# Kernel optimization log

Hardware: AMD Instinct MI355X
Metric: run time of the kernel (lower is better)

Reference implementation:

```python
import jax, jax.numpy as jnp
import numpy as np

N, E, B = 50000, 200000, 512
F0, H1, C2, EMB = 78, 10, 128, 128
SEQ, VOCAB, NF, KW = 1000, 26, 32, 8
LOUT = EMB - KW + 1  # 121


def setup_inputs() -> dict:
    key = jax.random.key(0)
    ks = jax.random.split(key, 20)
    nrm = lambda k, s: jax.random.normal(k, s, jnp.float32) * 0.05
    return dict(
        x=jax.random.normal(ks[0], (N, F0), jnp.float32),
        edge_index=jax.random.randint(ks[1], (2, E), 0, N),
        batch=(jnp.arange(N) * B) // N,  # balanced sorted node->graph ids, all segments non-empty
        target=jax.random.randint(ks[2], (B, SEQ), 0, VOCAB),
        W1=nrm(ks[3], (F0, H1 * F0)), a_src1=nrm(ks[4], (H1, F0)), a_dst1=nrm(ks[5], (H1, F0)), b1=jnp.zeros((H1 * F0,), jnp.float32),
        W2=nrm(ks[6], (H1 * F0, C2)), a_src2=nrm(ks[7], (1, C2)), a_dst2=nrm(ks[8], (1, C2)), b2=jnp.zeros((C2,), jnp.float32),
        fc_g1_w=nrm(ks[9], (C2, C2)), fc_g1_b=jnp.zeros((C2,), jnp.float32),
        emb=nrm(ks[10], (VOCAB, EMB)),
        conv_w=nrm(ks[11], (NF, SEQ, KW)), conv_b=jnp.zeros((NF,), jnp.float32),
        fc_xt_w=nrm(ks[12], (NF * LOUT, C2)), fc_xt_b=jnp.zeros((C2,), jnp.float32),
        fc1_w=nrm(ks[13], (2 * C2, 1024)), fc1_b=jnp.zeros((1024,), jnp.float32),
        fc2_w=nrm(ks[14], (1024, 256)), fc2_b=jnp.zeros((256,), jnp.float32),
        out_w=nrm(ks[15], (256, 1)), out_b=jnp.zeros((1,), jnp.float32),
    )


def gat_conv(x, src, dst, W, a_src, a_dst, b, heads):
    # PyG GATConv (eval mode): project, per-edge attn logits, segment softmax over dst, scatter-add
    n = x.shape[0]
    c = W.shape[1] // heads
    h = (x @ W).reshape(n, heads, c)                 # [N,H,C]
    al_s = (h * a_src).sum(-1)                       # [N,H]
    al_d = (h * a_dst).sum(-1)
    al = jax.nn.leaky_relu(al_s[src] + al_d[dst], 0.2)   # [E',H]
    amax = jax.ops.segment_max(al, dst, num_segments=n)
    ex = jnp.exp(al - amax[dst])
    den = jax.ops.segment_sum(ex, dst, num_segments=n)
    alpha = ex / (den[dst] + 1e-16)
    out = jax.ops.segment_sum(h[src] * alpha[:, :, None], dst, num_segments=n)  # [N,H,C]
    return out.reshape(n, heads * c) + b


def reference(x, edge_index, batch, target, W1, a_src1, a_dst1, b1, W2, a_src2, a_dst2, b2,
              fc_g1_w, fc_g1_b, emb, conv_w, conv_b, fc_xt_w, fc_xt_b,
              fc1_w, fc1_b, fc2_w, fc2_b, out_w, out_b):
    n = x.shape[0]
    loops = jnp.arange(n)
    src = jnp.concatenate([edge_index[0], loops])    # add self loops (PyG default)
    dst = jnp.concatenate([edge_index[1], loops])
    h = jax.nn.elu(gat_conv(x, src, dst, W1, a_src1, a_dst1, b1, H1))
    h = jax.nn.relu(gat_conv(h, src, dst, W2, a_src2, a_dst2, b2, 1))
    g = jax.ops.segment_max(h, batch, num_segments=B)            # global max pool per graph
    g = jax.nn.relu(g @ fc_g1_w + fc_g1_b)                       # [B,128]
    e = emb[target]                                              # [B,1000,128]
    conv = jax.lax.conv_general_dilated(e, conv_w, (1,), 'VALID',
                                        dimension_numbers=('NCH', 'OIH', 'NCH'))
    conv = jax.nn.relu(conv + conv_b[None, :, None])             # [B,32,121]
    xt = conv.reshape(B, NF * LOUT) @ fc_xt_w + fc_xt_b          # [B,128]
    xc = jnp.concatenate([g, xt], axis=1)                        # [B,256]
    xc = jax.nn.relu(xc @ fc1_w + fc1_b)
    xc = jax.nn.relu(xc @ fc2_w + fc2_b)
    return xc @ out_w + out_b                                    # [B,1]
```

## Files before the change

### kernel.cpp

```cpp
#include <hip/hip_runtime.h>
#include <hip/hip_bf16.h>

#define N_NODES 50000
#define N_EDGES 200000
#define BGRAPHS 512
#define F0c 78
#define H1c 10
#define HC1 780
#define HSTR 832
#define C2c 128
#define SEQc 1000
#define VOCABc 26
#define NFc 32
#define KWc 8
#define LOUTc 121
#define EMBc 128
#define KX 96
#define KXT 3872
#define MROWS 13312
#define KM 1024
#define W2TF_N (25*8*64*8)
#define NSCANB 196

typedef __attribute__((ext_vector_type(8))) short short8;
typedef __attribute__((ext_vector_type(4))) float f32x4;
typedef unsigned short u16;

static constexpr size_t alignup(size_t x) { return (x + 255) & ~size_t(255); }

static constexpr size_t A_HBUF = 0;
static constexpr size_t A_OUT1 = alignup(A_HBUF + size_t(N_NODES)*HSTR*2);
static constexpr size_t A_H2   = alignup(A_OUT1 + size_t(N_NODES)*HSTR*2);
static constexpr size_t A_W2T  = alignup(A_H2   + size_t(N_NODES)*C2c*4);
static constexpr size_t A_ALS1 = alignup(A_W2T  + size_t(C2c)*HSTR*2);
static constexpr size_t A_ALD1 = alignup(A_ALS1 + size_t(N_NODES)*H1c*4);
static constexpr size_t A_ALS2 = alignup(A_ALD1 + size_t(N_NODES)*H1c*4);
static constexpr size_t A_ALD2 = alignup(A_ALS2 + size_t(N_NODES)*4);
static constexpr size_t A_DEG  = alignup(A_ALD2 + size_t(N_NODES)*4);
static constexpr size_t A_OFFS = alignup(A_DEG  + size_t(N_NODES)*4);
static constexpr size_t A_CUR  = alignup(A_OFFS + size_t(N_NODES+1)*4);
static constexpr size_t A_CSRC = alignup(A_CUR  + size_t(N_NODES)*4);
static constexpr size_t A_XC   = alignup(A_CSRC + size_t(N_EDGES+N_NODES)*4);
static constexpr size_t A_Y1   = alignup(A_XC   + size_t(BGRAPHS)*256*4);
static constexpr size_t A_BOFF = alignup(A_Y1   + size_t(BGRAPHS)*1024*4);
static constexpr size_t A_BPAD = alignup(A_BOFF + size_t(BGRAPHS)*(VOCABc+1)*4);
static constexpr size_t A_WXT  = alignup(A_BPAD + size_t(HSTR)*4);
static constexpr size_t A_FXP  = alignup(A_WXT  + size_t(C2c)*KXT*2);
static constexpr size_t A_W1HP = alignup(A_FXP  + size_t(11)*BGRAPHS*C2c*4);
static constexpr size_t A_WSD  = alignup(A_W1HP + size_t(10)*80*96*2);
static constexpr size_t A_CWT  = alignup(A_WSD  + size_t(2)*H1c*F0c*4);
static constexpr size_t A_END  = alignup(A_CWT  + size_t(2)*256*KM*2);
static_assert(W2TF_N*2 <= size_t(C2c)*HSTR*2, "w2tf fits old slot");
static_assert((NSCANB+1)*4 <= BGRAPHS*(VOCABc+1)*4, "bsum fits A_BOFF slot");

static constexpr size_t A_HFIN = A_HBUF;
static constexpr size_t A_AMAT = alignup(A_HFIN + size_t(N_NODES)*C2c*4);
static constexpr size_t A_CVO  = alignup(A_AMAT + size_t(MROWS)*256*4);
static constexpr size_t A_M    = alignup(A_CVO  + size_t(BGRAPHS)*KXT*2);
static_assert(A_M + size_t(MROWS)*KM*2 <= size_t(N_NODES)*HSTR*2, "alias A overflow");
static constexpr size_t A_XPAD = A_OUT1;
static_assert(size_t(N_NODES)*KX*2 <= size_t(N_NODES)*HSTR*2, "alias B overflow");

__device__ __forceinline__ float bflo(unsigned u) { return __uint_as_float(u << 16); }
__device__ __forceinline__ float bfhi(unsigned u) { return __uint_as_float(u & 0xffff0000u); }
__device__ __forceinline__ u16 f2bf(float v) {
    __hip_bfloat16 b = __float2bfloat16(v);
    return *(u16*)&b;
}

#define GLOAD16(g, l) __builtin_amdgcn_global_load_lds( \
    (const __attribute__((address_space(1))) void*)(g), \
    (__attribute__((address_space(3))) void*)(l), 16, 0, 0)

__global__ void k_prep(const float* __restrict__ x, const float* __restrict__ W1,
                       const float* __restrict__ W2, const float* __restrict__ b1,
                       const float* __restrict__ fcxt_w, const float* __restrict__ conv_w,
                       const float* __restrict__ a_src1, const float* __restrict__ a_dst1,
                       __hip_bfloat16* __restrict__ xpad, __hip_bfloat16* __restrict__ w1hp,
                       u16* __restrict__ w2tf, float* __restrict__ bpad,
                       u16* __restrict__ wxt, float* __restrict__ wsd,
                       u16* __restrict__ cwt, int* __restrict__ deg) {
    int i = blockIdx.x*256 + threadIdx.x;
    const int R0 = N_NODES;
    const int R1 = R0 + N_NODES*KX;
    const int R2 = R1 + 10*80*96;
    const int R3 = R2 + W2TF_N;
    const int R4 = R3 + HSTR;
    const int R5 = R4 + C2c*KXT;
    const int R6 = R5 + 2*H1c*F0c;
    const int R7 = R6 + 256*KM;
    if (i < R0) {
        deg[i] = 1;
    } else if (i < R1) {
        int t = i - R0; int n = t / KX, c = t - n*KX;
        xpad[t] = __float2bfloat16(c < F0c ? x[(size_t)n*F0c + c] : 0.f);
    } else if (i < R2) {
        int t = i - R1; int hh = t / 7680, rem = t - hh*7680;
        int j = rem / 96, k = rem - j*96;
        w1hp[t] = __float2bfloat16((j < F0c && k < F0c) ? W1[(size_t)k*HC1 + hh*F0c + j] : 0.f);
    } else if (i < R3) {
        int t = i - R2; int frag = t >> 3, tt = t & 7;
        int m16 = frag & 15, quad = (frag >> 4) & 3, cbg = (frag >> 6) & 7, kstep = frag >> 9;
        int col = cbg*16 + m16;
        int k = kstep*32 + quad*8 + tt;
        int hh = k / 80, cc = k - hh*80;
        w2tf[t] = f2bf((cc < F0c) ? W2[(size_t)(hh*F0c + cc)*C2c + col] : 0.f);
    } else if (i < R4) {
        int p = i - R3; int hh = p / 80, cc = p - hh*80;
        bpad[p] = (hh < H1c && cc < F0c) ? b1[hh*F0c + cc] : 0.f;
    } else if (i < R5) {
        int t = i - R4; int frag = t >> 3, tt = t & 7;
        int lane = frag & 63, m16 = lane & 15, quad = lane >> 4;
        int ct = (frag >> 6) & 7, kt = frag >> 9;
        wxt[t] = f2bf(fcxt_w[(size_t)(kt*32 + quad*8 + tt)*C2c + (ct*16 + m16)]);
    } else if (i < R6) {
        int t = i - R5; int sd = t / (H1c*F0c), rem = t - sd*(H1c*F0c);
        int hh = rem / F0c, c = rem - hh*F0c;
        const float* a = sd ? a_dst1 : a_src1;
        float v = 0.f;
        for (int j = 0; j < F0c; j++) v += W1[(size_t)c*HC1 + hh*F0c + j] * a[hh*F0c + j];
        wsd[t] = v;
    } else if (i < R7) {
        int t = i - R6; int col = t >> 10, ii = t & (KM-1);
        int o = col >> 3, k = col & 7;
        float v = (ii < SEQc) ? conv_w[((size_t)o*SEQc + ii)*KWc + k] : 0.f;
        u16 h = f2bf(v);
        float hv = __uint_as_float((unsigned)h << 16);
        cwt[(size_t)col*KM + ii] = h;
        cwt[(size_t)256*KM + (size_t)col*KM + ii] = f2bf(v - hv);
    }
}
#define PREP_TOTAL (N_NODES + N_NODES*KX + 10*80*96 + W2TF_N + HSTR + C2c*KXT + 2*H1c*F0c + 256*KM)

__global__ void k_count(const int* __restrict__ ei, int* deg) {
    int i = blockIdx.x*256 + threadIdx.x;
    if (i < N_EDGES) atomicAdd(&deg[ei[N_EDGES + i]], 1);
}
__global__ void k_scan1(const int* __restrict__ deg, int* __restrict__ offs,
                        int* __restrict__ bsum, int n) {
    int b = blockIdx.x, tid = threadIdx.x, lane = tid & 63, wid = tid >> 6;
    int i = b*256 + tid;
    int v0 = (i < n) ? deg[i] : 0;
    int v = v0;
    for (int d = 1; d < 64; d <<= 1) { int t = __shfl_up(v, d, 64); if (lane >= d) v += t; }
    __shared__ int ws[4];
    if (lane == 63) ws[wid] = v;
    __syncthreads();
    if (tid == 0) {
        int r = 0;
        #pragma unroll
        for (int w = 0; w < 4; w++) { int t = ws[w]; ws[w] = r; r += t; }
        bsum[b] = r;
    }
    __syncthreads();
    if (i < n) offs[i] = ws[wid] + (v - v0);
}
__global__ void k_scan2(int* __restrict__ bsum, int nb) {
    __shared__ int s[NSCANB];
    int tid = threadIdx.x;
    for (int i = tid; i < nb; i += 256) s[i] = bsum[i];
    __syncthreads();
    if (tid == 0) {
        int r = 0;
        for (int b = 0; b < nb; b++) { int t = s[b]; s[b] = r; r += t; }
        bsum[nb] = r;
    }
    __syncthreads();
    for (int i = tid; i < nb; i += 256) bsum[i] = s[i];
}
__global__ void k_scan3(const int* __restrict__ bsum, int* __restrict__ offs,
                        int* __restrict__ cur, int n, int nb) {
    int b = blockIdx.x, i = b*256 + threadIdx.x;
    if (i < n) {
        int o = offs[i] + bsum[b];
        offs[i] = o; cur[i] = o;
    } else if (i == n) {
        offs[n] = bsum[nb];
    }
}
__global__ void k_fill(const int* __restrict__ ei, int* cur, int* __restrict__ csrc) {
    int i = blockIdx.x*256 + threadIdx.x;
    if (i < N_EDGES) {
        int s = ei[i], d = ei[N_EDGES + i];
        int p = atomicAdd(&cur[d], 1);
        csrc[p] = s;
    } else if (i < N_EDGES + N_NODES) {
        int n = i - N_EDGES;
        int p = atomicAdd(&cur[n], 1);
        csrc[p] = n;
    }
}
__global__ void k_sortcsr(const int* __restrict__ offs, int* __restrict__ csrc) {
    int n = blockIdx.x*256 + threadIdx.x;
    if (n >= N_NODES) return;
    int s = offs[n], e = offs[n+1];
    for (int i = s + 1; i < e; i++) {
        int v = csrc[i];
        int j = i - 1;
        while (j >= s && csrc[j] > v) { csrc[j+1] = csrc[j]; j--; }
        csrc[j+1] = v;
    }
}

__global__ void k_att1x(const float* __restrict__ x, const float* __restrict__ wsd,
                        float* __restrict__ als, float* __restrict__ ald) {
    int i = blockIdx.x*256 + threadIdx.x;
    if (i >= N_NODES*H1c) return;
    int n = i / H1c, hh = i - n*H1c;
    const float* xr = x + (size_t)n*F0c;
    const float* ws = wsd + hh*F0c;
    const float* wd = wsd + H1c*F0c + hh*F0c;
    float s1 = 0.f, s2 = 0.f;
    for (int c = 0; c < F0c; c++) { float v = xr[c]; s1 += v*ws[c]; s2 += v*wd[c]; }
    als[i] = s1; ald[i] = s2;
}

__global__ void k_agg1x(const unsigned* __restrict__ xpu, const float* __restrict__ als,
                        const float* __restrict__ ald, const int* __restrict__ offs,
                        const int* __restrict__ csrc, unsigned* __restrict__ xaggu) {
    constexpr int H = H1c;
    int dn = blockIdx.x, lane = threadIdx.x;
    int s = offs[dn], e = offs[dn+1], deg = e - s;
    __shared__ float wexp[64*H];
    __shared__ int   ssrc[64];
    __shared__ float ms[H], dinv_s[H];

    if (deg <= 64) {
        if (lane < deg) ssrc[lane] = csrc[s + lane];
        __syncthreads();
        for (int idx = lane; idx < deg*H; idx += 64) {
            int j = idx / H, hh = idx - j*H;
            float al = als[(size_t)ssrc[j]*H + hh] + ald[(size_t)dn*H + hh];
            wexp[idx] = (al >= 0.f) ? al : 0.2f*al;
        }
        __syncthreads();
        if (lane < H) {
            float m = -1e30f;
            for (int j = 0; j < deg; j++) m = fmaxf(m, wexp[j*H + lane]);
            float den = 0.f;
            for (int j = 0; j < deg; j++) den += __expf(wexp[j*H + lane] - m);
            ms[lane] = m; dinv_s[lane] = 1.f/(den + 1e-16f);
        }
        __syncthreads();
        for (int idx = lane; idx < deg*H; idx += 64) {
            int hh = idx % H;
            wexp[idx] = __expf(wexp[idx] - ms[hh]) * dinv_s[hh];
        }
        __syncthreads();
        if (lane < 40) {
            float accL[H], accH[H];
            #pragma unroll
            for (int hh = 0; hh < H; hh++) { accL[hh] = 0.f; accH[hh] = 0.f; }
            int j = 0;
            for (; j + 1 < deg; j += 2) {
                unsigned ua = xpu[(size_t)ssrc[j]*48 + lane];
                unsigned ub = xpu[(size_t)ssrc[j+1]*48 + lane];
                float a0 = bflo(ua), a1 = bfhi(ua), b0 = bflo(ub), b1 = bfhi(ub);
                #pragma unroll
                for (int hh = 0; hh < H; hh++) {
                    float wA = wexp[j*H + hh], wB = wexp[(j+1)*H + hh];
                    accL[hh] += wA*a0 + wB*b0;
                    accH[hh] += wA*a1 + wB*b1;
                }
            }
            if (j < deg) {
                unsigned ua = xpu[(size_t)ssrc[j]*48 + lane];
                float a0 = bflo(ua), a1 = bfhi(ua);
                #pragma unroll
                for (int hh = 0; hh < H; hh++) {
                    float wA = wexp[j*H + hh];
                    accL[hh] += wA*a0;
                    accH[hh] += wA*a1;
                }
            }
            #pragma unroll
            for (int hh = 0; hh < H; hh++) {
                unsigned p = (unsigned)f2bf(accL[hh]) | ((unsigned)f2bf(accH[hh]) << 16);
                xaggu[((size_t)dn*H + hh)*40 + lane] = p;
            }
        }
    } else {
        if (lane < H) {
            float adv = ald[(size_t)dn*H + lane];
            float m = -1e30f;
            for (int j = s; j < e; j++) {
                float al = als[(size_t)csrc[j]*H + lane] + adv;
                al = (al >= 0.f) ? al : 0.2f*al;
                m = fmaxf(m, al);
            }
            float den = 0.f;
            for (int j = s; j < e; j++) {
                float al = als[(size_t)csrc[j]*H + lane] + adv;
                al = (al >= 0.f) ? al : 0.2f*al;
                den += __expf(al - m);
            }
            ms[lane] = m; dinv_s[lane] = 1.f/(den + 1e-16f);
        }
        __syncthreads();
        if (lane < 40) {
            float accL[H], accH[H];
            #pragma unroll
            for (int hh = 0; hh < H; hh++) { accL[hh] = 0.f; accH[hh] = 0.f; }
            for (int j = s; j < e; j++) {
                int sj = csrc[j];
                unsigned ua = xpu[(size_t)sj*48 + lane];
                float a0 = bflo(ua), a1 = bfhi(ua);
                #pragma unroll
                for (int hh = 0; hh < H; hh++) {
                    float al = als[(size_t)sj*H + hh] + ald[(size_t)dn*H + hh];
                    al = (al >= 0.f) ? al : 0.2f*al;
                    float a = __expf(al - ms[hh]) * dinv_s[hh];
                    accL[hh] += a*a0;
                    accH[hh] += a*a1;
                }
            }
            #pragma unroll
            for (int hh = 0; hh < H; hh++) {
                unsigned p = (unsigned)f2bf(accL[hh]) | ((unsigned)f2bf(accH[hh]) << 16);
                xaggu[((size_t)dn*H + hh)*40 + lane] = p;
            }
        }
    }
}

__global__ void __launch_bounds__(256, 8)
k_fuse12(const short* __restrict__ xagg, const short* __restrict__ w1hp,
         const float* __restrict__ bpad, const short* __restrict__ w2tf,
         const float* __restrict__ a_src2, const float* __restrict__ a_dst2,
         float* __restrict__ Cout, float* __restrict__ als2, float* __restrict__ ald2) {
    __shared__ __attribute__((aligned(16))) short As[16*832];
    int tid = threadIdx.x;
    int wave = tid >> 6, lane = tid & 63;
    int m16 = lane & 15, quad = lane >> 4;
    int blockrow = blockIdx.x * 16;

    {
        int hg = wave;
        int rowc = min(blockrow + m16, N_NODES-1);
        for (int hh = hg; hh < H1c; hh += 4) {
            const short8* arow = (const short8*)(xagg + ((size_t)rowc*H1c + hh)*80);
            f32x4 acc1[5];
            #pragma unroll
            for (int ct = 0; ct < 5; ct++) acc1[ct] = (f32x4){0.f,0.f,0.f,0.f};
            #pragma unroll
            for (int kt = 0; kt < 3; kt++) {
                short8 af = arow[kt*4 + quad];
                #pragma unroll
                for (int ct = 0; ct < 5; ct++) {
                    const short8* brow = (const short8*)(w1hp + (size_t)(hh*80 + ct*16 + m16)*96);
                    acc1[ct] = __builtin_amdgcn_mfma_f32_16x16x32_bf16(af, brow[kt*4 + quad],
                                                                      acc1[ct], 0, 0, 0);
                }
            }
            #pragma unroll
            for (int ct = 0; ct < 5; ct++) {
                int col = hh*80 + ct*16 + m16;
                float bv = bpad[col];
                #pragma unroll
                for (int r = 0; r < 4; r++) {
                    int rl = quad*4 + r;
                    float v = acc1[ct][r] + bv;
                    v = (v > 0.f) ? v : (__expf(v) - 1.f);
                    *(u16*)((char*)As + rl*1664 + ((col*2) ^ ((rl & 7) << 4))) = f2bf(v);
                }
            }
        }
    }
    __syncthreads();

    int cg = wave;
    f32x4 acc[2];
    acc[0] = (f32x4){0.f,0.f,0.f,0.f};
    acc[1] = (f32x4){0.f,0.f,0.f,0.f};
    int S = (m16 & 7) << 4;
    const char* asRow = (const char*)As + (size_t)m16*1664;
    const short8* bp = (const short8*)w2tf;
    #pragma unroll 5
    for (int kstep = 0; kstep < 25; kstep++) {
        short8 af = *(const short8*)(asRow + ((kstep*64 + quad*16) ^ S));
        short8 b0 = bp[(size_t)(kstep*8 + cg*2    )*64 + lane];
        short8 b1 = bp[(size_t)(kstep*8 + cg*2 + 1)*64 + lane];
        acc[0] = __builtin_amdgcn_mfma_f32_16x16x32_bf16(af, b0, acc[0], 0, 0, 0);
        acc[1] = __builtin_amdgcn_mfma_f32_16x16x32_bf16(af, b1, acc[1], 0, 0, 0);
    }

    float asv[2], adv[2];
    #pragma unroll
    for (int ct = 0; ct < 2; ct++) {
        asv[ct] = a_src2[cg*32 + ct*16 + m16];
        adv[ct] = a_dst2[cg*32 + ct*16 + m16];
    }
    #pragma unroll
    for (int ct = 0; ct < 2; ct++) {
        int col = cg*32 + ct*16 + m16;
        #pragma unroll
        for (int r = 0; r < 4; r++) {
            int orow = blockrow + quad*4 + r;
            if (orow < N_NODES) Cout[(size_t)orow*C2c + col] = acc[ct][r];
        }
    }

    __syncthreads();
    float* sred  = (float*)As;
    float* sredd = sred + 64;
    #pragma unroll
    for (int r = 0; r < 4; r++) {
        float s1 = 0.f, s2 = 0.f;
        #pragma unroll
        for (int ct = 0; ct < 2; ct++) { s1 += acc[ct][r]*asv[ct]; s2 += acc[ct][r]*adv[ct]; }
        #pragma unroll
        for (int d = 1; d < 16; d <<= 1) { s1 += __shfl_xor(s1, d, 64); s2 += __shfl_xor(s2, d, 64); }
        if (m16 == 0) {
            int rl = quad*4 + r;
            sred[rl*4 + cg] = s1;
            sredd[rl*4 + cg] = s2;
        }
    }
    __syncthreads();
    if (tid < 16) {
        int orow = blockrow + tid;
        if (orow < N_NODES) {
            als2[orow] = sred[tid*4+0] + sred[tid*4+1] + sred[tid*4+2] + sred[tid*4+3];
            ald2[orow] = sredd[tid*4+0] + sredd[tid*4+1] + sredd[tid*4+2] + sredd[tid*4+3];
        }
    }
}

__global__ void k_agg2(const float* __restrict__ h2, const float* __restrict__ als,
                       const float* __restrict__ ald, const int* __restrict__ offs,
                       const int* __restrict__ csrc, const float* __restrict__ b2,
                       float* __restrict__ out) {
    int dn = blockIdx.x, lane = threadIdx.x;
    int s = offs[dn], e = offs[dn+1], deg = e - s;
    __shared__ float wexp[128];
    __shared__ int ssrc[128];

    if (deg <= 128) {
        float adv = ald[dn];
        for (int j = lane; j < deg; j += 64) {
            int sj = csrc[s + j];
            ssrc[j] = sj;
            float al = als[sj] + adv;
            wexp[j] = (al >= 0.f) ? al : 0.2f*al;
        }
        __syncthreads();
        float m = -1e30f;
        for (int j = lane; j < deg; j += 64) m = fmaxf(m, wexp[j]);
        #pragma unroll
        for (int d = 32; d > 0; d >>= 1) m = fmaxf(m, __shfl_xor(m, d, 64));
        __syncthreads();
        float den = 0.f;
        for (int j = lane; j < deg; j += 64) {
            float ex = __expf(wexp[j] - m);
            wexp[j] = ex;
            den += ex;
        }
        #pragma unroll
        for (int d = 32; d > 0; d >>= 1) den += __shfl_xor(den, d, 64);
        float dinv = 1.f/(den + 1e-16f);
        __syncthreads();
        float2 acc = {0.f, 0.f};
        for (int j = 0; j < deg; j++) {
            float alpha = wexp[j] * dinv;
            float2 v = ((const float2*)(h2 + (size_t)ssrc[j]*C2c))[lane];
            acc.x += alpha*v.x; acc.y += alpha*v.y;
        }
        float2 o;
        o.x = fmaxf(acc.x + b2[2*lane], 0.f);
        o.y = fmaxf(acc.y + b2[2*lane+1], 0.f);
        ((float2*)(out + (size_t)dn*C2c))[lane] = o;
    } else {
        __shared__ float sm[2];
        if (lane == 0) {
            float adv = ald[dn];
            float m = -1e30f;
            for (int j = s; j < e; j++) {
                float al = als[csrc[j]] + adv;
                al = (al >= 0.f) ? al : 0.2f*al;
                m = fmaxf(m, al);
            }
            float den = 0.f;
            for (int j = s; j < e; j++) {
                float al = als[csrc[j]] + adv;
                al = (al >= 0.f) ? al : 0.2f*al;
                den += __expf(al - m);
            }
            sm[0] = m; sm[1] = 1.f/(den + 1e-16f);
        }
        __syncthreads();
        float m = sm[0], dinv = sm[1], adv = ald[dn];
        float2 acc = {0.f, 0.f};
        for (int j = s; j < e; j++) {
            int sj = csrc[j];
            float al = als[sj] + adv;
            al = (al >= 0.f) ? al : 0.2f*al;
            float alpha = __expf(al - m) * dinv;
            float2 v = ((const float2*)(h2 + (size_t)sj*C2c))[lane];
            acc.x += alpha*v.x; acc.y += alpha*v.y;
        }
        float2 o;
        o.x = fmaxf(acc.x + b2[2*lane], 0.f);
        o.y = fmaxf(acc.y + b2[2*lane+1], 0.f);
        ((float2*)(out + (size_t)dn*C2c))[lane] = o;
    }
}

__global__ void k_poolfcg(const float* __restrict__ hf, const int* __restrict__ batch,
                          const float* __restrict__ W, const float* __restrict__ bias,
                          float* __restrict__ xc) {
    int b = blockIdx.x, tid = threadIdx.x;
    __shared__ int se[2];
    __shared__ float gs[C2c];
    if (tid < 2) {
        int key = b + tid;
        int lo = 0, hi = N_NODES;
        while (lo < hi) { int mid = (lo+hi) >> 1; if (batch[mid] < key) lo = mid+1; else hi = mid; }
        se[tid] = lo;
    }
    __syncthreads();
    int s = se[0], e = se[1];
    float m = -1e30f;
    for (int n = s; n < e; n++) m = fmaxf(m, hf[(size_t)n*C2c + tid]);
    gs[tid] = m;
    __syncthreads();
    float acc = bias[tid];
    for (int k = 0; k < C2c; k++) acc += gs[k] * W[k*C2c + tid];
    xc[b*256 + tid] = fmaxf(acc, 0.f);
}

__global__ void k_buildM(const int* __restrict__ target, u16* __restrict__ Mm) {
    int b = blockIdx.x, tid = threadIdx.x;
    short8 z = (short8){0,0,0,0,0,0,0,0};
    short8* base = (short8*)(Mm + (size_t)b*VOCABc*KM);
    for (int i = tid; i < VOCABc*KM/8; i += 256) base[i] = z;
    __syncthreads();
    for (int i = tid; i < SEQc; i += 256) {
        int t = target[(size_t)b*SEQc + i];
        Mm[((size_t)b*VOCABc + t)*KM + i] = (u16)0x3F80;
    }
}

__global__ void __launch_bounds__(256, 1)
k_amat_mfma(const short* __restrict__ Mm, const short* __restrict__ cwt,
            float* __restrict__ A2) {
    __shared__ __attribute__((aligned(16))) short As[2][128*64];
    __shared__ __attribute__((aligned(16))) short Bh[2][128*64];
    __shared__ __attribute__((aligned(16))) short Bl[2][128*64];
    int tid = threadIdx.x;
    int wave = tid >> 6, lane = tid & 63;
    int m16 = lane & 15, quad = lane >> 4;
    int blockrow = blockIdx.x * 128;
    int colbase  = blockIdx.y * 128;

    size_t aoff[4], bo[4];
    #pragma unroll
    for (int i = 0; i < 4; i++) {
        int c = wave*256 + i*64 + lane;
        int row = c >> 3;
        int cb  = (c & 7) << 4;
        int srcb = cb ^ ((row & 7) << 4);
        aoff[i] = (size_t)(blockrow + row) * (KM*2) + srcb;
        bo[i]   = (size_t)(colbase  + row) * (KM*2) + srcb;
    }
    const char* hbase = (const char*)cwt;
    const char* lbase = (const char*)(cwt + (size_t)256*KM);

    f32x4 acc[2][8];
    #pragma unroll
    for (int wr = 0; wr < 2; wr++)
        #pragma unroll
        for (int ct = 0; ct < 8; ct++) acc[wr][ct] = (f32x4){0.f,0.f,0.f,0.f};

    #pragma unroll
    for (int i = 0; i < 4; i++) {
        GLOAD16((const char*)Mm + aoff[i], &As[0][(wave*256 + i*64)*8]);
        GLOAD16(hbase + bo[i],             &Bh[0][(wave*256 + i*64)*8]);
        GLOAD16(lbase + bo[i],             &Bl[0][(wave*256 + i*64)*8]);
    }
    __syncthreads();

    int cur = 0;
    int S = (m16 & 7) << 4;
    for (int s = 0; s < KM/64; s++) {
        if (s + 1 < KM/64) {
            size_t kb = (size_t)(s + 1) * 128;
            #pragma unroll
            for (int i = 0; i < 4; i++) {
                GLOAD16((const char*)Mm + aoff[i] + kb, &As[cur^1][(wave*256 + i*64)*8]);
                GLOAD16(hbase + bo[i] + kb,             &Bh[cur^1][(wave*256 + i*64)*8]);
                GLOAD16(lbase + bo[i] + kb,             &Bl[cur^1][(wave*256 + i*64)*8]);
            }
        }
        const char* asBase = (const char*)&As[cur][0];
        const char* bhBase = (const char*)&Bh[cur][0];
        const char* blBase = (const char*)&Bl[cur][0];
        #pragma unroll
        for (int kk = 0; kk < 2; kk++) {
            int kb2 = (kk*64 + quad*16) ^ S;
            short8 af[2];
            #pragma unroll
            for (int wr = 0; wr < 2; wr++) {
                int row = wave*32 + wr*16 + m16;
                af[wr] = *(const short8*)(asBase + row*128 + kb2);
            }
            #pragma unroll
            for (int ct = 0; ct < 8; ct++) {
                int col = ct*16 + m16;
                short8 bhv = *(const short8*)(bhBase + col*128 + kb2);
                short8 blv = *(const short8*)(blBase + col*128 + kb2);
                acc[0][ct] = __builtin_amdgcn_mfma_f32_16x16x32_bf16(af[0], bhv, acc[0][ct], 0, 0, 0);
                acc[1][ct] = __builtin_amdgcn_mfma_f32_16x16x32_bf16(af[1], bhv, acc[1][ct], 0, 0, 0);
                acc[0][ct] = __builtin_amdgcn_mfma_f32_16x16x32_bf16(af[0], blv, acc[0][ct], 0, 0, 0);
                acc[1][ct] = __builtin_amdgcn_mfma_f32_16x16x32_bf16(af[1], blv, acc[1][ct], 0, 0, 0);
            }
        }
        __syncthreads();
        cur ^= 1;
    }

    #pragma unroll
    for (int wr = 0; wr < 2; wr++) {
        int rowbase = blockrow + wave*32 + wr*16 + quad*4;
        #pragma unroll
        for (int ct = 0; ct < 8; ct++) {
            int col = colbase + ct*16 + m16;
            #pragma unroll
            for (int r = 0; r < 4; r++) {
                A2[(size_t)(rowbase + r)*256 + col] = acc[wr][ct][r];
            }
        }
    }
}

__global__ void __launch_bounds__(128, 4)
k_conv(const float* __restrict__ A2, const float* __restrict__ emb,
       const float* __restrict__ convb, u16* __restrict__ convout) {
    int b = blockIdx.x, og = blockIdx.y;
    int tid = threadIdx.x;
    __shared__ float embs[VOCABc*EMBc];
    __shared__ float arow[4*VOCABc*KWc];
    for (int i = tid; i < VOCABc*EMBc; i += 128) embs[i] = emb[i];
    for (int i = tid; i < 4*VOCABc*KWc; i += 128) {
        int o2 = i / (VOCABc*KWc);
        int rem = i - o2*(VOCABc*KWc);
        int t = rem >> 3, k = rem & 7;
        arow[i] = A2[((size_t)b*VOCABc + t)*256 + (og*4 + o2)*8 + k];
    }
    __syncthreads();
    if (tid < LOUTc) {
        float a0 = convb[og*4+0], a1 = convb[og*4+1], a2 = convb[og*4+2], a3 = convb[og*4+3];
        for (int t = 0; t < VOCABc; t++) {
            #pragma unroll
            for (int k = 0; k < KWc; k++) {
                float ev = embs[t*EMBc + tid + k];
                a0 += arow[0*(VOCABc*KWc) + t*KWc + k] * ev;
                a1 += arow[1*(VOCABc*KWc) + t*KWc + k] * ev;
                a2 += arow[2*(VOCABc*KWc) + t*KWc + k] * ev;
                a3 += arow[3*(VOCABc*KWc) + t*KWc + k] * ev;
            }
        }
        size_t base = (size_t)b*KXT + (og*4)*LOUTc + tid;
        convout[base            ] = f2bf(fmaxf(a0, 0.f));
        convout[base +   LOUTc  ] = f2bf(fmaxf(a1, 0.f));
        convout[base + 2*LOUTc  ] = f2bf(fmaxf(a2, 0.f));
        convout[base + 3*LOUTc  ] = f2bf(fmaxf(a3, 0.f));
    }
}
__global__ void k_fcxt_mfma(const short* __restrict__ cvo, const short* __restrict__ wxt,
                            float* __restrict__ fxp) {
    int wave = threadIdx.x >> 6, lane = threadIdx.x & 63;
    int m16 = lane & 15, quad = lane >> 4;
    int r0 = blockIdx.x*64 + wave*16;
    int kt0 = blockIdx.y*11;
    const short8* arow = (const short8*)(cvo + (size_t)(r0 + m16)*KXT);
    const short8* bp = (const short8*)wxt;
    f32x4 acc[8];
    #pragma unroll
    for (int ct = 0; ct < 8; ct++) acc[ct] = (f32x4){0.f,0.f,0.f,0.f};
    for (int kt = kt0; kt < kt0 + 11; kt++) {
        short8 af = arow[kt*4 + quad];
        #pragma unroll
        for (int ct = 0; ct < 8; ct++) {
            short8 bf = bp[(size_t)(kt*8 + ct)*64 + lane];
            acc[ct] = __builtin_amdgcn_mfma_f32_16x16x32_bf16(af, bf, acc[ct], 0, 0, 0);
        }
    }
    #pragma unroll
    for (int ct = 0; ct < 8; ct++) {
        int col = ct*16 + m16;
        #pragma unroll
        for (int r = 0; r < 4; r++) {
            int row = r0 + quad*4 + r;
            fxp[((size_t)blockIdx.y*BGRAPHS + row)*C2c + col] = acc[ct][r];
        }
    }
}

__global__ void __launch_bounds__(256, 4)
k_fc1(const float* __restrict__ xc, const float* __restrict__ fxp,
      const float* __restrict__ fcxt_b, const float* __restrict__ W,
      const float* __restrict__ bias, float* __restrict__ y1) {
    int g0 = blockIdx.x * 8;
    int colq = blockIdx.y;
    int tid = threadIdx.x;
    __shared__ float xs[8][256];
    for (int idx = tid; idx < 8*256; idx += 256) {
        int g = idx >> 8, k = idx & 255;
        int b = g0 + g;
        float v;
        if (k < 128) {
            v = xc[b*256 + k];
        } else {
            int col = k - 128;
            float s = fcxt_b[col];
            #pragma unroll
            for (int q = 0; q < 11; q++) s += fxp[((size_t)q*BGRAPHS + b)*C2c + col];
            v = s;
        }
        xs[g][k] = v;
    }
    __syncthreads();
    int col = colq*256 + tid;
    float a[8];
    #pragma unroll
    for (int g = 0; g < 8; g++) a[g] = bias[col];
    for (int k = 0; k < 256; k++) {
        float w = W[(size_t)k*1024 + col];
        #pragma unroll
        for (int g = 0; g < 8; g++) a[g] += xs[g][k] * w;
    }
    #pragma unroll
    for (int g = 0; g < 8; g++)
        y1[(size_t)(g0+g)*1024 + col] = fmaxf(a[g], 0.f);
}
__global__ void __launch_bounds__(256, 4)
k_fc2out(const float* __restrict__ y1, const float* __restrict__ W,
         const float* __restrict__ bias, const float* __restrict__ ow,
         const float* __restrict__ ob, float* __restrict__ out) {
    int g0 = blockIdx.x * 2;
    int tid = threadIdx.x;
    int lane = tid & 63, wid = tid >> 6;
    __shared__ float ys[2][1024];
    __shared__ float wsum[2][4];
    for (int i = tid; i < 2048; i += 256)
        ys[i >> 10][i & 1023] = y1[(size_t)(g0 + (i >> 10))*1024 + (i & 1023)];
    __syncthreads();
    float acc0 = bias[tid], acc1 = bias[tid];
    for (int k = 0; k < 1024; k++) {
        float w = W[(size_t)k*256 + tid];
        acc0 += ys[0][k] * w;
        acc1 += ys[1][k] * w;
    }
    float v0 = fmaxf(acc0, 0.f) * ow[tid];
    float v1 = fmaxf(acc1, 0.f) * ow[tid];
    #pragma unroll
    for (int d = 32; d > 0; d >>= 1) { v0 += __shfl_xor(v0, d, 64); v1 += __shfl_xor(v1, d, 64); }
    if (lane == 0) { wsum[0][wid] = v0; wsum[1][wid] = v1; }
    __syncthreads();
    if (tid < 2)
        out[g0 + tid] = wsum[tid][0] + wsum[tid][1] + wsum[tid][2] + wsum[tid][3] + ob[0];
}

extern "C" void kernel_launch(void* const* d_in, const int* in_sizes, int n_in,
                              void* d_out, int out_size, void* d_ws, size_t ws_size,
                              hipStream_t stream) {
    (void)in_sizes; (void)n_in; (void)out_size;
    if (ws_size < A_END) return;

    const float* x       = (const float*)d_in[0];
    const int*   ei      = (const int*)  d_in[1];
    const int*   batch   = (const int*)  d_in[2];
    const int*   target  = (const int*)  d_in[3];
    const float* W1      = (const float*)d_in[4];
    const float* a_src1  = (const float*)d_in[5];
    const float* a_dst1  = (const float*)d_in[6];
    const float* b1      = (const float*)d_in[7];
    const float* W2      = (const float*)d_in[8];
    const float* a_src2  = (const float*)d_in[9];
    const float* a_dst2  = (const float*)d_in[10];
    const float* b2      = (const float*)d_in[11];
    const float* fcg_w   = (const float*)d_in[12];
    const float* fcg_b   = (const float*)d_in[13];
    const float* emb     = (const float*)d_in[14];
    const float* conv_w  = (const float*)d_in[15];
    const float* conv_b  = (const float*)d_in[16];
    const float* fcxt_w  = (const float*)d_in[17];
    const float* fcxt_b  = (const float*)d_in[18];
    const float* fc1_w   = (const float*)d_in[19];
    const float* fc1_b   = (const float*)d_in[20];
    const float* fc2_w   = (const float*)d_in[21];
    const float* fc2_b   = (const float*)d_in[22];
    const float* out_w   = (const float*)d_in[23];
    const float* out_b   = (const float*)d_in[24];

    char* wsb = (char*)d_ws;
    u16*   xagg  = (u16*)  (wsb + A_HBUF);
    float* h2    = (float*)(wsb + A_H2);
    u16*   w2tf  = (u16*)  (wsb + A_W2T);
    float* als1  = (float*)(wsb + A_ALS1);
    float* ald1  = (float*)(wsb + A_ALD1);
    float* als2  = (float*)(wsb + A_ALS2);
    float* ald2  = (float*)(wsb + A_ALD2);
    int*   deg   = (int*)  (wsb + A_DEG);
    int*   offs  = (int*)  (wsb + A_OFFS);
    int*   cur   = (int*)  (wsb + A_CUR);
    int*   csrc  = (int*)  (wsb + A_CSRC);
    float* xc    = (float*)(wsb + A_XC);
    float* y1    = (float*)(wsb + A_Y1);
    int*   bsum  = (int*)  (wsb + A_BOFF);
    float* bpad  = (float*)(wsb + A_BPAD);
    u16*   wxt   = (u16*)  (wsb + A_WXT);
    float* fxp   = (float*)(wsb + A_FXP);
    __hip_bfloat16* w1hp = (__hip_bfloat16*)(wsb + A_W1HP);
    float* wsd   = (float*)(wsb + A_WSD);
    u16*   cwt   = (u16*)  (wsb + A_CWT);
    float* hfin  = (float*)(wsb + A_HFIN);
    float* Amat2 = (float*)(wsb + A_AMAT);
    u16*   cvo   = (u16*)  (wsb + A_CVO);
    u16*   Mm    = (u16*)  (wsb + A_M);
    __hip_bfloat16* xpad = (__hip_bfloat16*)(wsb + A_XPAD);

    k_prep<<<(PREP_TOTAL+255)/256, 256, 0, stream>>>(x, W1, W2, b1, fcxt_w, conv_w,
                                                     a_src1, a_dst1,
                                                     xpad, w1hp, w2tf, bpad, wxt, wsd, cwt, deg);
    k_count  <<<(N_EDGES+255)/256, 256, 0, stream>>>(ei, deg);
    k_scan1  <<<NSCANB, 256, 0, stream>>>(deg, offs, bsum, N_NODES);
    k_scan2  <<<1, 256, 0, stream>>>(bsum, NSCANB);
    k_scan3  <<<NSCANB, 256, 0, stream>>>(bsum, offs, cur, N_NODES, NSCANB);
    k_fill   <<<(N_EDGES+N_NODES+255)/256, 256, 0, stream>>>(ei, cur, csrc);
    k_sortcsr<<<(N_NODES+255)/256, 256, 0, stream>>>(offs, csrc);

    k_att1x<<<(N_NODES*H1c+255)/256, 256, 0, stream>>>(x, wsd, als1, ald1);
    k_agg1x<<<N_NODES, 64, 0, stream>>>((const unsigned*)xpad, als1, ald1, offs, csrc,
                                        (unsigned*)xagg);

    k_fuse12<<<(N_NODES+15)/16, 256, 0, stream>>>((const short*)xagg, (const short*)w1hp,
                                                  bpad, (const short*)w2tf,
                                                  a_src2, a_dst2, h2, als2, ald2);

    k_buildM<<<BGRAPHS, 256, 0, stream>>>(target, Mm);

    k_agg2<<<N_NODES, 64, 0, stream>>>(h2, als2, ald2, offs, csrc, b2, hfin);

    k_poolfcg<<<BGRAPHS, 128, 0, stream>>>(hfin, batch, fcg_w, fcg_b, xc);

    k_amat_mfma<<<dim3(MROWS/128, 2), 256, 0, stream>>>((const short*)Mm, (const short*)cwt,
                                                        Amat2);
    k_conv  <<<dim3(BGRAPHS, 8), 128, 0, stream>>>(Amat2, emb, conv_b, cvo);
    k_fcxt_mfma<<<dim3(BGRAPHS/64, 11), 256, 0, stream>>>((const short*)cvo, (const short*)wxt, fxp);

    k_fc1<<<dim3(BGRAPHS/8, 4), 256, 0, stream>>>(xc, fxp, fcxt_b, fc1_w, fc1_b, y1);
    k_fc2out<<<BGRAPHS/2, 256, 0, stream>>>(y1, fc2_w, fc2_b, out_w, out_b, (float*)d_out);
}
```

Measured before the change: 502.2 us.

## Fuse layer-1 attention aggregation into projection GEMM kernel via LDS staging

Merges the per-node GAT layer-1 aggregation kernel into the fused W1/W2 MFMA kernel. Each wave aggregates four destination rows and writes the bf16 results into a swizzled shared-memory tile, which the GEMM stage then reads directly. This removes the global round trip of the aggregated [N,10,80] bf16 buffer and one kernel launch. In exchange, the kernel uses more LDS per block (occupancy target lowered from 8 to 4) and the aggregation runs on 4 rows per wave serially, with skewed degree distribution possibly creating imbalance across waves.

```diff
diff --git a/kernel.cpp b/kernel.cpp
--- a/kernel.cpp
+++ b/kernel.cpp
@@ -67,6 +67,7 @@
     __hip_bfloat16 b = __float2bfloat16(v);
     return *(u16*)&b;
 }
+#define WSYNC() __builtin_amdgcn_wave_barrier()
 
 #define GLOAD16(g, l) __builtin_amdgcn_global_load_lds( \
     (const __attribute__((address_space(1))) void*)(g), \
@@ -215,136 +216,146 @@
     als[i] = s1; ald[i] = s2;
 }
 
-__global__ void k_agg1x(const unsigned* __restrict__ xpu, const float* __restrict__ als,
-                        const float* __restrict__ ald, const int* __restrict__ offs,
-                        const int* __restrict__ csrc, unsigned* __restrict__ xaggu) {
+__global__ void __launch_bounds__(256, 4)
+k_fuse012(const unsigned* __restrict__ xpu, const float* __restrict__ als,
+          const float* __restrict__ ald, const int* __restrict__ offs,
+          const int* __restrict__ csrc,
+          const short* __restrict__ w1hp, const float* __restrict__ bpad,
+          const short* __restrict__ w2tf,
+          const float* __restrict__ a_src2, const float* __restrict__ a_dst2,
+          float* __restrict__ Cout, float* __restrict__ als2, float* __restrict__ ald2) {
     constexpr int H = H1c;
-    int dn = blockIdx.x, lane = threadIdx.x;
-    int s = offs[dn], e = offs[dn+1], deg = e - s;
-    __shared__ float wexp[64*H];
-    __shared__ int   ssrc[64];
-    __shared__ float ms[H], dinv_s[H];
-
-    if (deg <= 64) {
-        if (lane < deg) ssrc[lane] = csrc[s + lane];
-        __syncthreads();
-        for (int idx = lane; idx < deg*H; idx += 64) {
-            int j = idx / H, hh = idx - j*H;
-            float al = als[(size_t)ssrc[j]*H + hh] + ald[(size_t)dn*H + hh];
-            wexp[idx] = (al >= 0.f) ? al : 0.2f*al;
-        }
-        __syncthreads();
-        if (lane < H) {
-            float m = -1e30f;
-            for (int j = 0; j < deg; j++) m = fmaxf(m, wexp[j*H + lane]);
-            float den = 0.f;
-            for (int j = 0; j < deg; j++) den += __expf(wexp[j*H + lane] - m);
-            ms[lane] = m; dinv_s[lane] = 1.f/(den + 1e-16f);
-        }
-        __syncthreads();
-        for (int idx = lane; idx < deg*H; idx += 64) {
-            int hh = idx % H;
-            wexp[idx] = __expf(wexp[idx] - ms[hh]) * dinv_s[hh];
-        }
-        __syncthreads();
-        if (lane < 40) {
-            float accL[H], accH[H];
-            #pragma unroll
-            for (int hh = 0; hh < H; hh++) { accL[hh] = 0.f; accH[hh] = 0.f; }
-            int j = 0;
-            for (; j + 1 < deg; j += 2) {
-                unsigned ua = xpu[(size_t)ssrc[j]*48 + lane];
-                unsigned ub = xpu[(size_t)ssrc[j+1]*48 + lane];
-                float a0 = bflo(ua), a1 = bfhi(ua), b0 = bflo(ub), b1 = bfhi(ub);
-                #pragma unroll
-                for (int hh = 0; hh < H; hh++) {
-                    float wA = wexp[j*H + hh], wB = wexp[(j+1)*H + hh];
-                    accL[hh] += wA*a0 + wB*b0;
-                    accH[hh] += wA*a1 + wB*b1;
-                }
-            }
-            if (j < deg) {
-                unsigned ua = xpu[(size_t)ssrc[j]*48 + lane];
-                float a0 = bflo(ua), a1 = bfhi(ua);
-                #pragma unroll
-                for (int hh = 0; hh < H; hh++) {
-                    float wA = wexp[j*H + hh];
-                    accL[hh] += wA*a0;
-                    accH[hh] += wA*a1;
-                }
-            }
-            #pragma unroll
-            for (int hh = 0; hh < H; hh++) {
-                unsigned p = (unsigned)f2bf(accL[hh]) | ((unsigned)f2bf(accH[hh]) << 16);
-                xaggu[((size_t)dn*H + hh)*40 + lane] = p;
-            }
-        }
-    } else {
-        if (lane < H) {
-            float adv = ald[(size_t)dn*H + lane];
-            float m = -1e30f;
-            for (int j = s; j < e; j++) {
-                float al = als[(size_t)csrc[j]*H + lane] + adv;
-                al = (al >= 0.f) ? al : 0.2f*al;
-                m = fmaxf(m, al);
-            }
-            float den = 0.f;
-            for (int j = s; j < e; j++) {
-                float al = als[(size_t)csrc[j]*H + lane] + adv;
-                al = (al >= 0.f) ? al : 0.2f*al;
-                den += __expf(al - m);
-            }
-            ms[lane] = m; dinv_s[lane] = 1.f/(den + 1e-16f);
-        }
-        __syncthreads();
-        if (lane < 40) {
-            float accL[H], accH[H];
-            #pragma unroll
-            for (int hh = 0; hh < H; hh++) { accL[hh] = 0.f; accH[hh] = 0.f; }
-            for (int j = s; j < e; j++) {
-                int sj = csrc[j];
-                unsigned ua = xpu[(size_t)sj*48 + lane];
-                float a0 = bflo(ua), a1 = bfhi(ua);
-                #pragma unroll
-                for (int hh = 0; hh < H; hh++) {
-                    float al = als[(size_t)sj*H + hh] + ald[(size_t)dn*H + hh];
-                    al = (al >= 0.f) ? al : 0.2f*al;
-                    float a = __expf(al - ms[hh]) * dinv_s[hh];
-                    accL[hh] += a*a0;
-                    accH[hh] += a*a1;
-                }
-            }
-            #pragma unroll
-            for (int hh = 0; hh < H; hh++) {
-                unsigned p = (unsigned)f2bf(accL[hh]) | ((unsigned)f2bf(accH[hh]) << 16);
-                xaggu[((size_t)dn*H + hh)*40 + lane] = p;
-            }
-        }
-    }
-}
-
-__global__ void __launch_bounds__(256, 8)
-k_fuse12(const short* __restrict__ xagg, const short* __restrict__ w1hp,
-         const float* __restrict__ bpad, const short* __restrict__ w2tf,
-         const float* __restrict__ a_src2, const float* __restrict__ a_dst2,
-         float* __restrict__ Cout, float* __restrict__ als2, float* __restrict__ ald2) {
+    __shared__ __attribute__((aligned(16))) short Xs[16*832];
     __shared__ __attribute__((aligned(16))) short As[16*832];
     int tid = threadIdx.x;
     int wave = tid >> 6, lane = tid & 63;
     int m16 = lane & 15, quad = lane >> 4;
     int blockrow = blockIdx.x * 16;
 
+    float* wexp   = (float*)As + wave*(64*H);
+    int*   ssrc   = (int*)((char*)As + 10240) + wave*64;
+    float* ms     = (float*)((char*)As + 11264) + wave*H;
+    float* dinv_s = (float*)((char*)As + 11424) + wave*H;
+
+    for (int rr = 0; rr < 4; rr++) {
+        int rl = wave*4 + rr;
+        int dn = blockrow + rl;
+        int s = offs[dn], e = offs[dn+1], deg = e - s;
+        char* xrow = (char*)Xs + rl*1664;
+        int swz = (rl & 7) << 4;
+        if (lane < 32) *(unsigned*)(xrow + 1536 + lane*4) = 0u;
+        if (deg <= 64) {
+            if (lane < deg) ssrc[lane] = csrc[s + lane];
+            WSYNC();
+            for (int idx = lane; idx < deg*H; idx += 64) {
+                int j = idx / H, hh = idx - j*H;
+                float al = als[(size_t)ssrc[j]*H + hh] + ald[(size_t)dn*H + hh];
+                wexp[idx] = (al >= 0.f) ? al : 0.2f*al;
+            }
+            WSYNC();
+            if (lane < H) {
+                float m = -1e30f;
+                for (int j = 0; j < deg; j++) m = fmaxf(m, wexp[j*H + lane]);
+                float den = 0.f;
+                for (int j = 0; j < deg; j++) den += __expf(wexp[j*H + lane] - m);
+                ms[lane] = m; dinv_s[lane] = 1.f/(den + 1e-16f);
+            }
+            WSYNC();
+            for (int idx = lane; idx < deg*H; idx += 64) {
+                int hh = idx % H;
+                wexp[idx] = __expf(wexp[idx] - ms[hh]) * dinv_s[hh];
+            }
+            WSYNC();
+            if (lane < 40) {
+                float accL[H], accH[H];
+                #pragma unroll
+                for (int hh = 0; hh < H; hh++) { accL[hh] = 0.f; accH[hh] = 0.f; }
+                int j = 0;
+                for (; j + 1 < deg; j += 2) {
+                    unsigned ua = xpu[(size_t)ssrc[j]*48 + lane];
+                    unsigned ub = xpu[(size_t)ssrc[j+1]*48 + lane];
+                    float a0 = bflo(ua), a1 = bfhi(ua), b0 = bflo(ub), b1 = bfhi(ub);
+                    #pragma unroll
+                    for (int hh = 0; hh < H; hh++) {
+                        float wA = wexp[j*H + hh], wB = wexp[(j+1)*H + hh];
+                        accL[hh] += wA*a0 + wB*b0;
+                        accH[hh] += wA*a1 + wB*b1;
+                    }
+                }
+                if (j < deg) {
+                    unsigned ua = xpu[(size_t)ssrc[j]*48 + lane];
+                    float a0 = bflo(ua), a1 = bfhi(ua);
+                    #pragma unroll
+                    for (int hh = 0; hh < H; hh++) {
+                        float wA = wexp[j*H + hh];
+                        accL[hh] += wA*a0;
+                        accH[hh] += wA*a1;
+                    }
+                }
+                #pragma unroll
+                for (int hh = 0; hh < H; hh++) {
+                    unsigned p = (unsigned)f2bf(accL[hh]) | ((unsigned)f2bf(accH[hh]) << 16);
+                    *(unsigned*)(xrow + ((hh*160 + lane*4) ^ swz)) = p;
+                }
+            }
+            WSYNC();
+        } else {
+            if (lane < H) {
+                float adv = ald[(size_t)dn*H + lane];
+                float m = -1e30f;
+                for (int j = s; j < e; j++) {
+                    float al = als[(size_t)csrc[j]*H + lane] + adv;
+                    al = (al >= 0.f) ? al : 0.2f*al;
+                    m = fmaxf(m, al);
+                }
+                float den = 0.f;
+                for (int j = s; j < e; j++) {
+                    float al = als[(size_t)csrc[j]*H + lane] + adv;
+                    al = (al >= 0.f) ? al : 0.2f*al;
+                    den += __expf(al - m);
+                }
+                ms[lane] = m; dinv_s[lane] = 1.f/(den + 1e-16f);
+            }
+            WSYNC();
+            if (lane < 40) {
+                float accL[H], accH[H];
+                #pragma unroll
+                for (int hh = 0; hh < H; hh++) { accL[hh] = 0.f; accH[hh] = 0.f; }
+                for (int j = s; j < e; j++) {
+                    int sj = csrc[j];
+                    unsigned ua = xpu[(size_t)sj*48 + lane];
+                    float a0 = bflo(ua), a1 = bfhi(ua);
+                    #pragma unroll
+                    for (int hh = 0; hh < H; hh++) {
+                        float al = als[(size_t)sj*H + hh] + ald[(size_t)dn*H + hh];
+                        al = (al >= 0.f) ? al : 0.2f*al;
+                        float a = __expf(al - ms[hh]) * dinv_s[hh];
+                        accL[hh] += a*a0;
+                        accH[hh] += a*a1;
+                    }
+                }
+                #pragma unroll
+                for (int hh = 0; hh < H; hh++) {
+                    unsigned p = (unsigned)f2bf(accL[hh]) | ((unsigned)f2bf(accH[hh]) << 16);
+                    *(unsigned*)(xrow + ((hh*160 + lane*4) ^ swz)) = p;
+                }
+            }
+            WSYNC();
+        }
+    }
+    __syncthreads();
+
     {
         int hg = wave;
-        int rowc = min(blockrow + m16, N_NODES-1);
+        int S1 = (m16 & 7) << 4;
+        const char* xrowR = (const char*)Xs + m16*1664;
         for (int hh = hg; hh < H1c; hh += 4) {
-            const short8* arow = (const short8*)(xagg + ((size_t)rowc*H1c + hh)*80);
             f32x4 acc1[5];
             #pragma unroll
             for (int ct = 0; ct < 5; ct++) acc1[ct] = (f32x4){0.f,0.f,0.f,0.f};
             #pragma unroll
             for (int kt = 0; kt < 3; kt++) {
-                short8 af = arow[kt*4 + quad];
+                short8 af = *(const short8*)(xrowR + ((hh*160 + (kt*4 + quad)*16) ^ S1));
                 #pragma unroll
                 for (int ct = 0; ct < 5; ct++) {
                     const short8* brow = (const short8*)(w1hp + (size_t)(hh*80 + ct*16 + m16)*96);
@@ -396,7 +407,7 @@
         #pragma unroll
         for (int r = 0; r < 4; r++) {
             int orow = blockrow + quad*4 + r;
-            if (orow < N_NODES) Cout[(size_t)orow*C2c + col] = acc[ct][r];
+            Cout[(size_t)orow*C2c + col] = acc[ct][r];
         }
     }
 
@@ -419,10 +430,8 @@
     __syncthreads();
     if (tid < 16) {
         int orow = blockrow + tid;
-        if (orow < N_NODES) {
-            als2[orow] = sred[tid*4+0] + sred[tid*4+1] + sred[tid*4+2] + sred[tid*4+3];
-            ald2[orow] = sredd[tid*4+0] + sredd[tid*4+1] + sredd[tid*4+2] + sredd[tid*4+3];
-        }
+        als2[orow] = sred[tid*4+0] + sred[tid*4+1] + sred[tid*4+2] + sred[tid*4+3];
+        ald2[orow] = sredd[tid*4+0] + sredd[tid*4+1] + sredd[tid*4+2] + sredd[tid*4+3];
     }
 }
 
@@ -794,7 +803,6 @@
     const float* out_b   = (const float*)d_in[24];
 
     char* wsb = (char*)d_ws;
-    u16*   xagg  = (u16*)  (wsb + A_HBUF);
     float* h2    = (float*)(wsb + A_H2);
     u16*   w2tf  = (u16*)  (wsb + A_W2T);
     float* als1  = (float*)(wsb + A_ALS1);
@@ -831,12 +839,10 @@
     k_sortcsr<<<(N_NODES+255)/256, 256, 0, stream>>>(offs, csrc);
 
     k_att1x<<<(N_NODES*H1c+255)/256, 256, 0, stream>>>(x, wsd, als1, ald1);
-    k_agg1x<<<N_NODES, 64, 0, stream>>>((const unsigned*)xpad, als1, ald1, offs, csrc,
-                                        (unsigned*)xagg);
-
-    k_fuse12<<<(N_NODES+15)/16, 256, 0, stream>>>((const short*)xagg, (const short*)w1hp,
-                                                  bpad, (const short*)w2tf,
-                                                  a_src2, a_dst2, h2, als2, ald2);
+
+    k_fuse012<<<N_NODES/16, 256, 0, stream>>>((const unsigned*)xpad, als1, ald1, offs, csrc,
+                                              (const short*)w1hp, bpad, (const short*)w2tf,
+                                              a_src2, a_dst2, h2, als2, ald2);
 
     k_buildM<<<BGRAPHS, 256, 0, stream>>>(target, Mm);
 
```

Result: slower. 512.8 us (+2.1%).
